# Optimization experiments

Measured on AMD Instinct MI355X. Metric: run time of the kernel, lower is better.

The kernel has to match this reference:

```python
import jax, jax.numpy as jnp
import numpy as np

B, L, N = 8, 5, 4096
RADIUS, K = 0.7, 32
SPATIAL_STRIDE = 16
TK, TSTRIDE = 3, 2  # temporal kernel / stride; temporal_padding=[1,1] replicate
DIM, DEPTH, HEADS, DIM_HEAD, MLP_DIM, OUT_DIM = 512, 5, 8, 64, 1024, 1088
INNER = HEADS * DIM_HEAD
N_ANCH = 64
NTOT = N + N_ANCH
M = NTOT // SPATIAL_STRIDE  # spatial anchors per output frame


def setup_inputs() -> dict:
    key = jax.random.key(0)
    ks = list(jax.random.split(key, 16))
    s = 0.02
    p = {}
    p["points"] = jax.random.uniform(ks[0], (B, L, N, 3), jnp.float32, -1.0, 1.0)
    p["conv_d_w"] = jax.random.normal(ks[1], (DIM, 4), jnp.float32) * s
    p["conv_f_w"] = jax.random.normal(ks[2], (DIM, 3), jnp.float32) * s
    p["pos_w"] = jax.random.normal(ks[3], (DIM, 4), jnp.float32) * s
    p["pos_b"] = jnp.zeros((DIM,), jnp.float32)
    p["ln1_g"] = jnp.ones((DEPTH, DIM)); p["ln1_b"] = jnp.zeros((DEPTH, DIM))
    p["qkv_w"] = jax.random.normal(ks[4], (DEPTH, DIM, 3 * INNER), jnp.float32) * s
    p["attn_out_w"] = jax.random.normal(ks[5], (DEPTH, INNER, DIM), jnp.float32) * s
    p["attn_out_b"] = jnp.zeros((DEPTH, DIM))
    p["ln2_g"] = jnp.ones((DEPTH, DIM)); p["ln2_b"] = jnp.zeros((DEPTH, DIM))
    p["ff1_w"] = jax.random.normal(ks[6], (DEPTH, DIM, MLP_DIM), jnp.float32) * s
    p["ff1_b"] = jnp.zeros((DEPTH, MLP_DIM))
    p["ff2_w"] = jax.random.normal(ks[7], (DEPTH, MLP_DIM, DIM), jnp.float32) * s
    p["ff2_b"] = jnp.zeros((DEPTH, DIM))
    p["head_ln_g"] = jnp.ones((DIM,)); p["head_ln_b"] = jnp.zeros((DIM,))
    p["head1_w"] = jax.random.normal(ks[8], (DIM, MLP_DIM), jnp.float32) * s
    p["head1_b"] = jnp.zeros((MLP_DIM,))
    p["head2_w"] = jax.random.normal(ks[9], (MLP_DIM, OUT_DIM), jnp.float32) * s
    p["head2_b"] = jnp.zeros((OUT_DIM,))
    return p


def _layer_norm(x, g, b, eps=1e-5):
    mu = jnp.mean(x, -1, keepdims=True)
    var = jnp.mean((x - mu) ** 2, -1, keepdims=True)
    return (x - mu) * jax.lax.rsqrt(var + eps) * g + b


def _anchor_grid():
    lin = jnp.linspace(-1.5, 1.5, 4)
    gx, gy, gz = jnp.meshgrid(lin, lin, lin, indexing="ij")
    return jnp.stack([gx.ravel(), gy.ravel(), gz.ravel()], -1)  # (64,3)


def _fps(pts, m):
    # furthest point sampling, pts (N,3) -> (m,) int32, first pick is index 0 (pointnet2 semantics)
    def step(carry, _):
        dist, last = carry
        d = jnp.sum((pts - pts[last]) ** 2, -1)
        dist = jnp.minimum(dist, d)
        return (dist, jnp.argmax(dist).astype(jnp.int32)), last
    init = (jnp.full((pts.shape[0],), 1e10, pts.dtype), jnp.int32(0))
    _, idx = jax.lax.scan(step, init, None, length=m)
    return idx


def _ball_query(anchors, pts, radius, k):
    # first k point indices within radius of each anchor; pad with first hit (0 if none)
    d2 = jnp.sum((anchors[:, None, :] - pts[None, :, :]) ** 2, -1)  # (M,N)
    n = pts.shape[0]
    cand = jnp.where(d2 < radius * radius, jnp.arange(n, dtype=jnp.int32), n)
    neg_topk, _ = jax.lax.top_k(-cand, k)  # k smallest indices, ascending
    idx = -neg_topk
    first = idx[:, :1]
    idx = jnp.where(idx == n, first, idx)
    return jnp.where(idx == n, 0, idx)


def _forward(points, conv_d_w, conv_f_w, pos_w, pos_b, ln1_g, ln1_b, qkv_w,
             attn_out_w, attn_out_b, ln2_g, ln2_b, ff1_w, ff1_b, ff2_w, ff2_b,
             head_ln_g, head_ln_b, head1_w, head1_b, head2_w, head2_b):
    anch = _anchor_grid()  # (64,3)
    pts = jnp.concatenate(
        [points[..., :3], jnp.broadcast_to(anch, (B, L, N_ANCH, 3))], axis=2)  # (B,L,NTOT,3)
    # replicate temporal padding [1,1]
    frames = jnp.concatenate([pts[:, :1], pts, pts[:, -1:]], axis=1)  # (B,L+2,NTOT,3)

    trad = (TK - 1) // 2
    nT = L + 2
    gather = jax.vmap(lambda p, i: p[i])
    out_xyz, out_feat = [], []
    for t in range(trad, nT - trad, TSTRIDE):
        f_t = frames[:, t]                                   # (B,NTOT,3)
        a_idx = jax.vmap(lambda p: _fps(p, M))(f_t)          # (B,M)
        a_xyz = gather(f_t, a_idx)                           # (B,M,3)
        feats_w = []
        for i in range(t - trad, t + trad + 1):
            nb = frames[:, i]                                # (B,NTOT,3)
            idx = jax.vmap(lambda a, p: _ball_query(a, p, RADIUS, K))(a_xyz, nb)  # (B,M,K)
            grouped = gather(nb, idx)                        # (B,M,K,3)
            disp = grouped - a_xyz[:, :, None, :]
            tdisp = jnp.full((B, M, K, 1), float(i - t), disp.dtype)
            disp4 = jnp.concatenate([disp, tdisp], -1)       # (B,M,K,4)
            # conv_f(features) + conv_d(displacement); features fed in are the xyz themselves
            feat = (jnp.einsum("bmkc,dc->bmkd", grouped, conv_f_w)
                    + jnp.einsum("bmkc,dc->bmkd", disp4, conv_d_w))
            feats_w.append(jnp.max(feat, axis=2))            # spatial max -> (B,M,DIM)
        out_feat.append(jnp.max(jnp.stack(feats_w, 0), axis=0))  # temporal max
        out_xyz.append(a_xyz)

    nF = len(out_xyz)
    xyzs = jnp.stack(out_xyz, 1)                             # (B,nF,M,3)
    feats = jnp.stack(out_feat, 1).reshape(B, nF * M, DIM)
    tcol = jnp.broadcast_to(
        jnp.arange(1, nF + 1, dtype=xyzs.dtype)[None, :, None, None], (B, nF, M, 1))
    xyzts = jnp.concatenate([xyzs, tcol], -1).reshape(B, nF * M, 4)
    x = jnp.einsum("bnc,dc->bnd", xyzts, pos_w) + pos_b + feats  # (B,T,DIM); emb_relu=False

    scale = DIM_HEAD ** -0.5
    for l in range(DEPTH):
        xn = _layer_norm(x, ln1_g[l], ln1_b[l])
        q, k, v = jnp.split(xn @ qkv_w[l], 3, axis=-1)
        rs = lambda a: a.reshape(B, -1, HEADS, DIM_HEAD)
        q, k, v = rs(q), rs(k), rs(v)
        att = jax.nn.softmax(jnp.einsum("bqhd,bkhd->bhqk", q, k) * scale, axis=-1)
        o = jnp.einsum("bhqk,bkhd->bqhd", att, v).reshape(B, -1, INNER)
        x = x + o @ attn_out_w[l] + attn_out_b[l]
        xn = _layer_norm(x, ln2_g[l], ln2_b[l])
        x = x + jax.nn.gelu(xn @ ff1_w[l] + ff1_b[l], approximate=False) @ ff2_w[l] + ff2_b[l]

    x = jnp.max(x, axis=1)                                   # (B,DIM)
    x = _layer_norm(x, head_ln_g, head_ln_b)
    x = jax.nn.gelu(x @ head1_w + head1_b, approximate=False) @ head2_w + head2_b
    x = x.reshape(B, 1, OUT_DIM // 64, 64)
    x = jax.nn.softmax(x, axis=-1)
    return x @ anch                                          # (B,1,J,3)


def reference(points, conv_d_w, conv_f_w, pos_w, pos_b, ln1_g, ln1_b, qkv_w,
              attn_out_w, attn_out_b, ln2_g, ln2_b, ff1_w, ff1_b, ff2_w, ff2_b,
              head_ln_g, head_ln_b, head1_w, head1_b, head2_w, head2_b):
    return _forward(points, conv_d_w, conv_f_w, pos_w, pos_b, ln1_g, ln1_b, qkv_w,
                    attn_out_w, attn_out_b, ln2_g, ln2_b, ff1_w, ff1_b, ff2_w, ff2_b,
                    head_ln_g, head_ln_b, head1_w, head1_b, head2_w, head2_b)
```

## Files before the change

### kernel.cpp

```cpp
#include <hip/hip_runtime.h>
#include <hip/hip_bf16.h>
#include <cstddef>

#define BB 8
#define LL 5
#define NN 4096
#define NANCH 64
#define NPTS 4160
#define MM 260
#define NFRAME 3
#define SSEQ 780
#define DIMC 512
#define NHEAD 8
#define DHEAD 64
#define MLPD 1024
#define OUTD 1088
#define NROWS 6240
#define VPITCH 784
#define WBUFSZ 2097152

typedef __attribute__((ext_vector_type(8))) short s16x8;
typedef __attribute__((ext_vector_type(4))) float fx4;
typedef unsigned short ushort_t;
typedef unsigned int uint_t;

__device__ __forceinline__ float sqdist_rn(float x1, float y1, float z1,
                                           float x2, float y2, float z2) {
    float dx = __fsub_rn(x1, x2);
    float dy = __fsub_rn(y1, y2);
    float dz = __fsub_rn(z1, z2);
    return __fadd_rn(__fadd_rn(__fmul_rn(dx, dx), __fmul_rn(dy, dy)), __fmul_rn(dz, dz));
}

__device__ __forceinline__ float gelu_exact(float v) {
    return 0.5f * v * (1.0f + erff(v * 0.70710678118654752440f));
}

__device__ __forceinline__ uint_t bf16rn(float f) {
    uint_t u = __float_as_uint(f);
    return (u + 0x7FFFu + ((u >> 16) & 1u)) >> 16;
}
__device__ __forceinline__ void split2(float f, ushort_t& h, ushort_t& l) {
    uint_t hb = bf16rn(f);
    h = (ushort_t)hb;
    float fh = __uint_as_float(hb << 16);
    l = (ushort_t)bf16rn(f - fh);
}

template <int CTRL>
__device__ __forceinline__ int dpp_mov(int v) {
    return __builtin_amdgcn_update_dpp(0, v, CTRL, 0xF, 0xF, true);
}
#define DPP_STEP_F(op, v, ctrl) v = op(v, __int_as_float(dpp_mov<ctrl>(__float_as_int(v))))
__device__ __forceinline__ float wave_max_bcast(float v) {
    DPP_STEP_F(fmaxf, v, 0x111); DPP_STEP_F(fmaxf, v, 0x112);
    DPP_STEP_F(fmaxf, v, 0x114); DPP_STEP_F(fmaxf, v, 0x118);
    DPP_STEP_F(fmaxf, v, 0x142); DPP_STEP_F(fmaxf, v, 0x143);
    return __int_as_float(__builtin_amdgcn_readlane(__float_as_int(v), 63));
}
__device__ __forceinline__ float faddf(float a, float b) { return a + b; }
__device__ __forceinline__ float wave_sum_bcast(float v) {
    DPP_STEP_F(faddf, v, 0x111); DPP_STEP_F(faddf, v, 0x112);
    DPP_STEP_F(faddf, v, 0x114); DPP_STEP_F(faddf, v, 0x118);
    DPP_STEP_F(faddf, v, 0x142); DPP_STEP_F(faddf, v, 0x143);
    return __int_as_float(__builtin_amdgcn_readlane(__float_as_int(v), 63));
}
#define DPP_STEP_I(v, ctrl) { int _x = dpp_mov<ctrl>(v); v = v > _x ? v : _x; }
__device__ __forceinline__ int wave_maxi_bcast(int v) {
    DPP_STEP_I(v, 0x111); DPP_STEP_I(v, 0x112);
    DPP_STEP_I(v, 0x114); DPP_STEP_I(v, 0x118);
    DPP_STEP_I(v, 0x142); DPP_STEP_I(v, 0x143);
    return __builtin_amdgcn_readlane(v, 63);
}
__device__ __forceinline__ float row16_maxf(float v) {
    DPP_STEP_F(fmaxf, v, 0x111); DPP_STEP_F(fmaxf, v, 0x112);
    DPP_STEP_F(fmaxf, v, 0x114); DPP_STEP_F(fmaxf, v, 0x118);
    return __int_as_float(__builtin_amdgcn_readlane(__float_as_int(v), 15));
}
__device__ __forceinline__ int row16_maxi(int v) {
    DPP_STEP_I(v, 0x111); DPP_STEP_I(v, 0x112);
    DPP_STEP_I(v, 0x114); DPP_STEP_I(v, 0x118);
    return __builtin_amdgcn_readlane(v, 15);
}

__device__ __forceinline__ void wsplit_tile(
    int bid, int tid, int nthr,
    const float* __restrict__ qkvw, const float* __restrict__ projw,
    const float* __restrict__ ff1w, const float* __restrict__ ff2w,
    ushort_t* __restrict__ th, ushort_t* __restrict__ tl,
    float (*T)[33]) {
    const float* src; int K, N; size_t dst;
    if (bid < 768)       { src = qkvw;  K = 512;  N = 1536; dst = 0;       }
    else if (bid < 1024) { src = projw; K = 512;  N = 512;  dst = 786432;  bid -= 768;  }
    else if (bid < 1536) { src = ff1w;  K = 512;  N = 1024; dst = 1048576; bid -= 1024; }
    else                 { src = ff2w;  K = 1024; N = 512;  dst = 1572864; bid -= 1536; }
    int ntn = N >> 5;
    int tn = bid % ntn, tk = bid / ntn;
    int n0 = tn * 32, k0 = tk * 32;
    for (int e = tid; e < 1024; e += nthr) {
        int r = e >> 5, c = e & 31;
        T[r][c] = src[(size_t)(k0 + r) * N + n0 + c];
    }
    __syncthreads();
    for (int e = tid; e < 1024; e += nthr) {
        int r = e >> 5, c = e & 31;
        ushort_t h, l;
        split2(T[c][r], h, l);
        th[dst + (size_t)(n0 + r) * K + k0 + c] = h;
        tl[dst + (size_t)(n0 + r) * K + k0 + c] = l;
    }
}

__global__ __launch_bounds__(256) void build_pts_kernel(const float* __restrict__ points,
                                                        float* __restrict__ pts) {
    int i = blockIdx.x * 256 + threadIdx.x;
    if (i >= BB * LL * NPTS) return;
    int n = i % NPTS;
    int bl = i / NPTS;
    if (n < NN) {
        const float* src = points + ((size_t)bl * NN + n) * 3;
        pts[(size_t)i * 3 + 0] = src[0];
        pts[(size_t)i * 3 + 1] = src[1];
        pts[(size_t)i * 3 + 2] = src[2];
    } else {
        int j = n - NN;
        int ix = j >> 4, iy = (j >> 2) & 3, iz = j & 3;
        pts[(size_t)i * 3 + 0] = -1.5f + (float)ix;
        pts[(size_t)i * 3 + 1] = -1.5f + (float)iy;
        pts[(size_t)i * 3 + 2] = -1.5f + (float)iz;
    }
}

__global__ __launch_bounds__(1024) void fps_ws_kernel(
    const float* __restrict__ pts, float* __restrict__ axyz,
    const float* __restrict__ qkvw, const float* __restrict__ projw,
    const float* __restrict__ ff1w, const float* __restrict__ ff2w,
    ushort_t* __restrict__ th, ushort_t* __restrict__ tl) {
    __shared__ __align__(16) char smem[50432];
    int bid = blockIdx.x;
    int tid = threadIdx.x;
    if (bid >= 24) {
        wsplit_tile(bid - 24, tid, 1024, qkvw, projw, ff1w, ff2w, th, tl,
                    (float(*)[33])smem);
        return;
    }
    float* sx = (float*)smem;
    float* sy = sx + NPTS;
    float* sz = sy + NPTS;
    float* redv = sz + NPTS;
    int* redi = (int*)(redv + 32);

    int b = bid / 3, f = bid % 3;
    const float* P = pts + (size_t)(b * LL + 2 * f) * NPTS * 3;
    int lane = tid & 63, wid = tid >> 6;
    const int PPT = 5;
    float px[PPT], py[PPT], pz[PPT], dist[PPT];
#pragma unroll
    for (int j = 0; j < PPT; j++) {
        int n = tid + 1024 * j;
        if (n < NPTS) {
            float gx = P[(size_t)n * 3 + 0];
            float gy = P[(size_t)n * 3 + 1];
            float gz = P[(size_t)n * 3 + 2];
            px[j] = gx; py[j] = gy; pz[j] = gz;
            sx[n] = gx; sy[n] = gy; sz[n] = gz;
            dist[j] = 1e10f;
        } else {
            px[j] = 0.f; py[j] = 0.f; pz[j] = 0.f;
            dist[j] = -1.0f;
        }
    }
    __syncthreads();
    float ax = sx[0], ay = sy[0], az = sz[0];
    float* out = axyz + (size_t)bid * MM * 3;
    for (int m = 0; m < MM; m++) {
        if (tid == 0) { out[m * 3 + 0] = ax; out[m * 3 + 1] = ay; out[m * 3 + 2] = az; }
        float bestv = -1.0f;
        int bestn = NPTS;
#pragma unroll
        for (int j = 0; j < PPT; j++) {
            int n = tid + 1024 * j;
            if (n < NPTS) {
                float d = sqdist_rn(px[j], py[j], pz[j], ax, ay, az);
                float dj = fminf(dist[j], d);
                dist[j] = dj;
                if (dj > bestv) { bestv = dj; bestn = n; }
            }
        }
        float wm = wave_max_bcast(bestv);
        int wn = 0x7FFFFFFF - wave_maxi_bcast(bestv == wm ? (0x7FFFFFFF - bestn) : 0);
        int par = (m & 1) * 16;
        if (lane == 0) { redv[par + wid] = wm; redi[par + wid] = wn; }
        __syncthreads();
        float cv = redv[par + (lane & 15)];
        int ci = redi[par + (lane & 15)];
        float bv = row16_maxf(cv);
        int bn = 0x7FFFFFFF - row16_maxi(cv == bv ? (0x7FFFFFFF - ci) : 0);
        ax = sx[bn]; ay = sy[bn]; az = sz[bn];
    }
}

__global__ __launch_bounds__(64) void group_conv_kernel(
    const float* __restrict__ pts, const float* __restrict__ axyz,
    const float* __restrict__ conv_d_w, const float* __restrict__ conv_f_w,
    const float* __restrict__ pos_w, const float* __restrict__ pos_b,
    float* __restrict__ x) {
    int gid = blockIdx.x;
    int b = gid / SSEQ;
    int rem = gid % SSEQ;
    int f = rem / MM;
    int lane = threadIdx.x;
    const float* A = axyz + (size_t)gid * 3;
    float ax = A[0], ay = A[1], az = A[2];

    float cf0[8], cf1[8], cf2[8], cd0[8], cd1[8], cd2[8], cd3[8], fmx[8];
#pragma unroll
    for (int c = 0; c < 8; c++) {
        int d = lane + 64 * c;
        cf0[c] = conv_f_w[d * 3 + 0];
        cf1[c] = conv_f_w[d * 3 + 1];
        cf2[c] = conv_f_w[d * 3 + 2];
        cd0[c] = conv_d_w[d * 4 + 0];
        cd1[c] = conv_d_w[d * 4 + 1];
        cd2[c] = conv_d_w[d * 4 + 2];
        cd3[c] = conv_d_w[d * 4 + 3];
        fmx[c] = -INFINITY;
    }
    __shared__ int nbr[32];
    __shared__ float gxs[32], gys[32], gzs[32];
    const float R2 = 0.49000000953674316f;

    for (int wi = 0; wi < 3; wi++) {
        int l = 2 * f + wi - 1;
        l = l < 0 ? 0 : (l > 4 ? 4 : l);
        const float* P = pts + (size_t)(b * LL + l) * NPTS * 3;
        int cnt = 0;
        for (int base = 0; base < NPTS && cnt < 32; base += 64) {
            int n = base + lane;
            float d2 = sqdist_rn(P[(size_t)n * 3], P[(size_t)n * 3 + 1], P[(size_t)n * 3 + 2],
                                 ax, ay, az);
            bool hit = d2 < R2;
            unsigned long long mk = __ballot(hit);
            int rank = (int)__popcll(mk & (((unsigned long long)1 << lane) - 1ull));
            if (hit && (cnt + rank) < 32) nbr[cnt + rank] = n;
            cnt += (int)__popcll(mk);
        }
        __syncthreads();
        int eff = cnt < 32 ? cnt : 32;
        if (lane < 32) {
            int idx = (eff == 0) ? 0 : (lane < eff ? nbr[lane] : nbr[0]);
            gxs[lane] = P[(size_t)idx * 3 + 0];
            gys[lane] = P[(size_t)idx * 3 + 1];
            gzs[lane] = P[(size_t)idx * 3 + 2];
        }
        __syncthreads();
        float tf = (float)(wi - 1);
        for (int k = 0; k < 32; k++) {
            float gx = gxs[k], gy = gys[k], gz = gzs[k];
            float dx = gx - ax, dy = gy - ay, dz = gz - az;
#pragma unroll
            for (int c = 0; c < 8; c++) {
                float v = gx * cf0[c] + gy * cf1[c] + gz * cf2[c] +
                          dx * cd0[c] + dy * cd1[c] + dz * cd2[c] + tf * cd3[c];
                fmx[c] = fmaxf(fmx[c], v);
            }
        }
        __syncthreads();
    }
    float tcol = (float)(f + 1);
#pragma unroll
    for (int c = 0; c < 8; c++) {
        int d = lane + 64 * c;
        float pos = ax * pos_w[d * 4 + 0] + ay * pos_w[d * 4 + 1] +
                    az * pos_w[d * 4 + 2] + tcol * pos_w[d * 4 + 3] + pos_b[d];
        x[(size_t)gid * DIMC + d] = fmx[c] + pos;
    }
}

__global__ __launch_bounds__(64) void ln_kernel(const float* __restrict__ x,
                                                const float* __restrict__ g,
                                                const float* __restrict__ b,
                                                ushort_t* __restrict__ yh,
                                                ushort_t* __restrict__ yl) {
    int r = blockIdx.x;
    int lane = threadIdx.x;
    const float* xr = x + (size_t)r * DIMC;
    float4 v0 = *(const float4*)(xr + lane * 8);
    float4 v1 = *(const float4*)(xr + lane * 8 + 4);
    float s = v0.x + v0.y + v0.z + v0.w + v1.x + v1.y + v1.z + v1.w;
    s = wave_sum_bcast(s);
    float mean = s * (1.0f / 512.0f);
    float dv[8];
    dv[0] = v0.x - mean; dv[1] = v0.y - mean; dv[2] = v0.z - mean; dv[3] = v0.w - mean;
    dv[4] = v1.x - mean; dv[5] = v1.y - mean; dv[6] = v1.z - mean; dv[7] = v1.w - mean;
    float sq = 0.f;
#pragma unroll
    for (int c = 0; c < 8; c++) sq += dv[c] * dv[c];
    sq = wave_sum_bcast(sq);
    float var = sq * (1.0f / 512.0f);
    float inv = 1.0f / sqrtf(var + 1e-5f);
    int d = lane * 8;
    ushort_t hs[8], ls[8];
#pragma unroll
    for (int c = 0; c < 8; c++) {
        float v = dv[c] * inv * g[d + c] + b[d + c];
        split2(v, hs[c], ls[c]);
    }
    uint4 hv, lv;
    hv.x = hs[0] | ((uint_t)hs[1] << 16); hv.y = hs[2] | ((uint_t)hs[3] << 16);
    hv.z = hs[4] | ((uint_t)hs[5] << 16); hv.w = hs[6] | ((uint_t)hs[7] << 16);
    lv.x = ls[0] | ((uint_t)ls[1] << 16); lv.y = ls[2] | ((uint_t)ls[3] << 16);
    lv.z = ls[4] | ((uint_t)ls[5] << 16); lv.w = ls[6] | ((uint_t)ls[7] << 16);
    *(uint4*)(yh + (size_t)r * DIMC + d) = hv;
    *(uint4*)(yl + (size_t)r * DIMC + d) = lv;
}

#define KP 40

template <int BN, int EPI>
__global__ __launch_bounds__(256, 2) void gemm_mfma(
    const ushort_t* __restrict__ Ahg, const ushort_t* __restrict__ Alg,
    const ushort_t* __restrict__ Bhg, const ushort_t* __restrict__ Blg,
    const float* __restrict__ bias, const float* __restrict__ R,
    float* __restrict__ C, ushort_t* __restrict__ Ch, ushort_t* __restrict__ Cl,
    ushort_t* __restrict__ Vh, ushort_t* __restrict__ Vl,
    int M, int N, int K) {
    const int WN = BN / 2, NT = WN / 16;
    __shared__ ushort_t Ah[128 * KP];
    __shared__ ushort_t Al[128 * KP];
    __shared__ ushort_t Bh[BN * KP];
    __shared__ ushort_t Bl[BN * KP];
    int tid = threadIdx.x;
    int lane = tid & 63, w = tid >> 6;
    int wm = w & 1, wn = w >> 1;
    int quad = lane >> 4, l15 = lane & 15;
    int m0 = blockIdx.y * 128, n0 = blockIdx.x * BN;

    int sa_row = tid >> 2;
    int sa_k = (tid & 3) * 8;

    int row_a0 = m0 + sa_row;       if (row_a0 >= M) row_a0 = M - 1;
    int row_a1 = m0 + sa_row + 64;  if (row_a1 >= M) row_a1 = M - 1;
    const ushort_t* pAh0 = Ahg + (size_t)row_a0 * K + sa_k;
    const ushort_t* pAl0 = Alg + (size_t)row_a0 * K + sa_k;
    const ushort_t* pAh1 = Ahg + (size_t)row_a1 * K + sa_k;
    const ushort_t* pAl1 = Alg + (size_t)row_a1 * K + sa_k;
    const ushort_t* pBh0 = Bhg + (size_t)(n0 + sa_row) * K + sa_k;
    const ushort_t* pBl0 = Blg + (size_t)(n0 + sa_row) * K + sa_k;
    const ushort_t* pBh1 = (BN == 128) ? Bhg + (size_t)(n0 + sa_row + 64) * K + sa_k : pBh0;
    const ushort_t* pBl1 = (BN == 128) ? Blg + (size_t)(n0 + sa_row + 64) * K + sa_k : pBl0;

    fx4 acc[4][NT];
#pragma unroll
    for (int mi = 0; mi < 4; mi++)
#pragma unroll
        for (int nj = 0; nj < NT; nj++) acc[mi][nj] = (fx4){0.f, 0.f, 0.f, 0.f};

    float4 ra0h = *(const float4*)pAh0, ra0l = *(const float4*)pAl0;
    float4 ra1h = *(const float4*)pAh1, ra1l = *(const float4*)pAl1;
    float4 rb0h = *(const float4*)pBh0, rb0l = *(const float4*)pBl0;
    float4 rb1h, rb1l;
    if (BN == 128) { rb1h = *(const float4*)pBh1; rb1l = *(const float4*)pBl1; }

    for (int k0 = 0; k0 < K; k0 += 32) {
        *(float4*)&Ah[sa_row * KP + sa_k] = ra0h;
        *(float4*)&Al[sa_row * KP + sa_k] = ra0l;
        *(float4*)&Ah[(sa_row + 64) * KP + sa_k] = ra1h;
        *(float4*)&Al[(sa_row + 64) * KP + sa_k] = ra1l;
        *(float4*)&Bh[sa_row * KP + sa_k] = rb0h;
        *(float4*)&Bl[sa_row * KP + sa_k] = rb0l;
        if (BN == 128) {
            *(float4*)&Bh[(sa_row + 64) * KP + sa_k] = rb1h;
            *(float4*)&Bl[(sa_row + 64) * KP + sa_k] = rb1l;
        }
        __syncthreads();
        int kn = k0 + 32;
        if (kn < K) {
            ra0h = *(const float4*)(pAh0 + kn); ra0l = *(const float4*)(pAl0 + kn);
            ra1h = *(const float4*)(pAh1 + kn); ra1l = *(const float4*)(pAl1 + kn);
            rb0h = *(const float4*)(pBh0 + kn); rb0l = *(const float4*)(pBl0 + kn);
            if (BN == 128) {
                rb1h = *(const float4*)(pBh1 + kn); rb1l = *(const float4*)(pBl1 + kn);
            }
        }
        s16x8 af[4][2], bf[NT][2];
#pragma unroll
        for (int mi = 0; mi < 4; mi++) {
            int off = (64 * wm + 16 * mi + l15) * KP + quad * 8;
            af[mi][0] = *(const s16x8*)&Ah[off];
            af[mi][1] = *(const s16x8*)&Al[off];
        }
#pragma unroll
        for (int nj = 0; nj < NT; nj++) {
            int off = (WN * wn + 16 * nj + l15) * KP + quad * 8;
            bf[nj][0] = *(const s16x8*)&Bh[off];
            bf[nj][1] = *(const s16x8*)&Bl[off];
        }
#pragma unroll
        for (int mi = 0; mi < 4; mi++)
#pragma unroll
            for (int nj = 0; nj < NT; nj++) {
                acc[mi][nj] = __builtin_amdgcn_mfma_f32_16x16x32_bf16(af[mi][0], bf[nj][0], acc[mi][nj], 0, 0, 0);
                acc[mi][nj] = __builtin_amdgcn_mfma_f32_16x16x32_bf16(af[mi][0], bf[nj][1], acc[mi][nj], 0, 0, 0);
                acc[mi][nj] = __builtin_amdgcn_mfma_f32_16x16x32_bf16(af[mi][1], bf[nj][0], acc[mi][nj], 0, 0, 0);
            }
        __syncthreads();
    }
#pragma unroll
    for (int mi = 0; mi < 4; mi++) {
#pragma unroll
        for (int r = 0; r < 4; r++) {
            int row = m0 + 64 * wm + 16 * mi + quad * 4 + r;
            if (row < M) {
#pragma unroll
                for (int nj = 0; nj < NT; nj++) {
                    int col = n0 + WN * wn + 16 * nj + l15;
                    float v = acc[mi][nj][r];
                    if (EPI == 0) {
                        C[(size_t)row * N + col] = v;
                    } else if (EPI == 3) {
                        C[(size_t)row * N + col] = v + bias[col] + R[(size_t)row * N + col];
                    } else if (EPI == 2) {
                        float gv = gelu_exact(v + bias[col]);
                        ushort_t h, l;
                        split2(gv, h, l);
                        Ch[(size_t)row * N + col] = h;
                        Cl[(size_t)row * N + col] = l;
                    } else if (EPI == 5) {
                        ushort_t h, l;
                        split2(v, h, l);
                        if (col < 1024) {
                            Ch[(size_t)row * 1024 + col] = h;
                            Cl[(size_t)row * 1024 + col] = l;
                        } else {
                            int bb = row / SSEQ, key = row % SSEQ;
                            int hh = (col - 1024) >> 6, dd = (col - 1024) & 63;
                            size_t vo = ((size_t)((bb * 8 + hh) * 64 + dd)) * VPITCH + key;
                            Vh[vo] = h;
                            Vl[vo] = l;
                        }
                    }
                }
            }
        }
    }
}

#define AP 72

__global__ __launch_bounds__(256, 2) void attn_mfma_kernel(
    const ushort_t* __restrict__ qkh, const ushort_t* __restrict__ qkl,
    const ushort_t* __restrict__ vth, const ushort_t* __restrict__ vtl,
    ushort_t* __restrict__ oh, ushort_t* __restrict__ ol,
    const float* __restrict__ nqkvw, const float* __restrict__ nprojw,
    const float* __restrict__ nff1w, const float* __restrict__ nff2w,
    ushort_t* __restrict__ nth, ushort_t* __restrict__ ntl) {
    __shared__ __align__(16) char smem[73728];
    if (blockIdx.x >= 13) {
        int widx = (blockIdx.x - 13) * 64 + blockIdx.y * 8 + blockIdx.z;
        wsplit_tile(widx, threadIdx.x, 256, nqkvw, nprojw, nff1w, nff2w,
                    nth, ntl, (float(*)[33])smem);
        return;
    }
    ushort_t* Qh  = (ushort_t*)smem;
    ushort_t* Ql  = Qh + 64 * AP;
    ushort_t* Kh  = Ql + 64 * AP;
    ushort_t* Kl  = Kh + 64 * AP;
    ushort_t* Vth = Kl + 64 * AP;
    ushort_t* Vtl = Vth + 64 * AP;
    ushort_t* Ph  = Vtl + 64 * AP;
    ushort_t* Pl  = Ph + 64 * AP;

    int qt = blockIdx.x, h = blockIdx.y, b = blockIdx.z;
    int tid = threadIdx.x;
    int lane = tid & 63, w = tid >> 6;
    int quad = lane >> 4, l15 = lane & 15;
    int bh = b * 8 + h;

    int q0 = qt * 64;
    int nq = SSEQ - q0; if (nq > 64) nq = 64;

#pragma unroll
    for (int i = 0; i < 2; i++) {
        int t = tid + 256 * i;
        int row = t >> 3, c = (t & 7) * 8;
        int gq = q0 + (row < nq ? row : nq - 1);
        size_t go = (size_t)(b * SSEQ + gq) * 1024 + h * 64 + c;
        *(uint4*)&Qh[row * AP + c] = *(const uint4*)(qkh + go);
        *(uint4*)&Ql[row * AP + c] = *(const uint4*)(qkl + go);
    }

    fx4 accO[4];
#pragma unroll
    for (int dj = 0; dj < 4; dj++) accO[dj] = (fx4){0.f, 0.f, 0.f, 0.f};
    fx4 accL = (fx4){0.f, 0.f, 0.f, 0.f};

    s16x8 ones;
#pragma unroll
    for (int j = 0; j < 8; j++) ones[j] = (short)16256;

    for (int kt = 0; kt < 13; kt++) {
        int k0 = kt * 64;
        int nk = SSEQ - k0; if (nk > 64) nk = 64;
        __syncthreads();
#pragma unroll
        for (int i = 0; i < 2; i++) {
            int t = tid + 256 * i;
            int row = t >> 3, c = (t & 7) * 8;
            int gk = k0 + (row < nk ? row : nk - 1);
            size_t go = (size_t)(b * SSEQ + gk) * 1024 + h * 64 + c;
            *(uint4*)&Kh[row * AP + c] = *(const uint4*)(qkh + go + 512);
            *(uint4*)&Kl[row * AP + c] = *(const uint4*)(qkl + go + 512);
            size_t vo = ((size_t)(bh * 64 + row)) * VPITCH + k0 + c;
            *(uint4*)&Vth[row * AP + c] = *(const uint4*)(vth + vo);
            *(uint4*)&Vtl[row * AP + c] = *(const uint4*)(vtl + vo);
        }
        __syncthreads();

        fx4 accS[4];
#pragma unroll
        for (int nj = 0; nj < 4; nj++) accS[nj] = (fx4){0.f, 0.f, 0.f, 0.f};
#pragma unroll
        for (int ks = 0; ks < 2; ks++) {
            s16x8 aH = *(const s16x8*)&Qh[(16 * w + l15) * AP + 32 * ks + quad * 8];
            s16x8 aL = *(const s16x8*)&Ql[(16 * w + l15) * AP + 32 * ks + quad * 8];
#pragma unroll
            for (int nj = 0; nj < 4; nj++) {
                s16x8 bH = *(const s16x8*)&Kh[(16 * nj + l15) * AP + 32 * ks + quad * 8];
                s16x8 bL = *(const s16x8*)&Kl[(16 * nj + l15) * AP + 32 * ks + quad * 8];
                accS[nj] = __builtin_amdgcn_mfma_f32_16x16x32_bf16(aH, bH, accS[nj], 0, 0, 0);
                accS[nj] = __builtin_amdgcn_mfma_f32_16x16x32_bf16(aH, bL, accS[nj], 0, 0, 0);
                accS[nj] = __builtin_amdgcn_mfma_f32_16x16x32_bf16(aL, bH, accS[nj], 0, 0, 0);
            }
        }
#pragma unroll
        for (int nj = 0; nj < 4; nj++) {
            int key = 16 * nj + l15;
            bool valid = key < nk;
#pragma unroll
            for (int r = 0; r < 4; r++) {
                float s = accS[nj][r] * 0.125f;
                float p = valid ? __expf(s) : 0.f;
                ushort_t hh, ll;
                split2(p, hh, ll);
                int qrow = 16 * w + quad * 4 + r;
                Ph[qrow * AP + key] = hh;
                Pl[qrow * AP + key] = ll;
            }
        }
#pragma unroll
        for (int ks = 0; ks < 2; ks++) {
            s16x8 aPh = *(const s16x8*)&Ph[(16 * w + l15) * AP + 32 * ks + quad * 8];
            s16x8 aPl = *(const s16x8*)&Pl[(16 * w + l15) * AP + 32 * ks + quad * 8];
            accL = __builtin_amdgcn_mfma_f32_16x16x32_bf16(aPh, ones, accL, 0, 0, 0);
            accL = __builtin_amdgcn_mfma_f32_16x16x32_bf16(aPl, ones, accL, 0, 0, 0);
#pragma unroll
            for (int dj = 0; dj < 4; dj++) {
                s16x8 bVh = *(const s16x8*)&Vth[(16 * dj + l15) * AP + 32 * ks + quad * 8];
                s16x8 bVl = *(const s16x8*)&Vtl[(16 * dj + l15) * AP + 32 * ks + quad * 8];
                accO[dj] = __builtin_amdgcn_mfma_f32_16x16x32_bf16(aPh, bVh, accO[dj], 0, 0, 0);
                accO[dj] = __builtin_amdgcn_mfma_f32_16x16x32_bf16(aPh, bVl, accO[dj], 0, 0, 0);
                accO[dj] = __builtin_amdgcn_mfma_f32_16x16x32_bf16(aPl, bVh, accO[dj], 0, 0, 0);
            }
        }
    }
#pragma unroll
    for (int r = 0; r < 4; r++) {
        int lq = 16 * w + quad * 4 + r;
        if (lq < nq) {
            float inv = 1.0f / accL[r];
            size_t base = (size_t)(b * SSEQ + q0 + lq) * DIMC + h * 64 + l15;
#pragma unroll
            for (int dj = 0; dj < 4; dj++) {
                ushort_t hh, ll;
                split2(accO[dj][r] * inv, hh, ll);
                oh[base + 16 * dj] = hh;
                ol[base + 16 * dj] = ll;
            }
        }
    }
}

__global__ __launch_bounds__(512) void pool_max_kernel(const float* __restrict__ x,
                                                       float* __restrict__ partial) {
    int c = blockIdx.x;
    int bb = blockIdx.y;
    int d = threadIdx.x;
    const float* xb = x + ((size_t)(bb * SSEQ + c * 60)) * DIMC + d;
    float m = -INFINITY;
#pragma unroll 4
    for (int s = 0; s < 60; s++) m = fmaxf(m, xb[(size_t)s * DIMC]);
    partial[((size_t)bb * 13 + c) * DIMC + d] = m;
}

__global__ __launch_bounds__(512) void pool_ln_kernel(const float* __restrict__ partial,
                                                      const float* __restrict__ g,
                                                      const float* __restrict__ b,
                                                      float* __restrict__ out) {
    int bb = blockIdx.x;
    int d = threadIdx.x;
    const float* pb = partial + (size_t)bb * 13 * DIMC + d;
    float m = -INFINITY;
#pragma unroll
    for (int c = 0; c < 13; c++) m = fmaxf(m, pb[(size_t)c * DIMC]);
    __shared__ float col[512];
    __shared__ float red[512];
    col[d] = m;
    red[d] = m;
    __syncthreads();
    for (int s = 256; s > 0; s >>= 1) {
        if (d < s) red[d] += red[d + s];
        __syncthreads();
    }
    float mean = red[0] * (1.0f / 512.0f);
    __syncthreads();
    float dv = col[d] - mean;
    red[d] = dv * dv;
    __syncthreads();
    for (int s = 256; s > 0; s >>= 1) {
        if (d < s) red[d] += red[d + s];
        __syncthreads();
    }
    float var = red[0] * (1.0f / 512.0f);
    float inv = 1.0f / sqrtf(var + 1e-5f);
    out[(size_t)bb * DIMC + d] = dv * inv * g[d] + b[d];
}

__global__ __launch_bounds__(256) void head1_kernel(const float* __restrict__ in,
                                                    const float* __restrict__ W,
                                                    const float* __restrict__ bias,
                                                    float* __restrict__ out) {
    int g = blockIdx.x, bb = blockIdx.y;
    int tid = threadIdx.x;
    int c = tid & 63, ks = tid >> 6;
    int col = g * 64 + c;
    __shared__ float xr[512];
    xr[tid] = in[(size_t)bb * 512 + tid];
    xr[tid + 256] = in[(size_t)bb * 512 + tid + 256];
    __syncthreads();
    float acc = 0.f;
    const float* Wc = W + col;
    for (int k = ks * 128; k < ks * 128 + 128; k++)
        acc += xr[k] * Wc[(size_t)k * MLPD];
    __shared__ float red[256];
    red[tid] = acc;
    __syncthreads();
    if (ks == 0) {
        float v = red[c] + red[c + 64] + red[c + 128] + red[c + 192] + bias[col];
        out[(size_t)bb * MLPD + col] = gelu_exact(v);
    }
}

__global__ __launch_bounds__(256) void head2_kernel(const float* __restrict__ in,
                                                    const float* __restrict__ W,
                                                    const float* __restrict__ bias,
                                                    float* __restrict__ out) {
    int g = blockIdx.x, bb = blockIdx.y;
    int tid = threadIdx.x;
    int c = tid & 63, ks = tid >> 6;
    int col = g * 64 + c;
    __shared__ float xr[1024];
    xr[tid] = in[(size_t)bb * 1024 + tid];
    xr[tid + 256] = in[(size_t)bb * 1024 + tid + 256];
    xr[tid + 512] = in[(size_t)bb * 1024 + tid + 512];
    xr[tid + 768] = in[(size_t)bb * 1024 + tid + 768];
    __syncthreads();
    float acc = 0.f;
    const float* Wc = W + col;
    for (int k = ks * 256; k < ks * 256 + 256; k++)
        acc += xr[k] * Wc[(size_t)k * OUTD];
    __shared__ float red[256];
    red[tid] = acc;
    __syncthreads();
    if (ks == 0) {
        out[(size_t)bb * OUTD + col] = red[c] + red[c + 64] + red[c + 128] + red[c + 192] + bias[col];
    }
}

__global__ __launch_bounds__(64) void smax_anchor_kernel(const float* __restrict__ h2,
                                                         float* __restrict__ out) {
    int bb = blockIdx.x / 17;
    int gcol = blockIdx.x % 17;
    int j = threadIdx.x;
    float v = h2[(size_t)bb * OUTD + gcol * 64 + j];
    float mx = wave_max_bcast(v);
    float p = expf(v - mx);
    float sum = wave_sum_bcast(p);
    int ix = j >> 4, iy = (j >> 2) & 3, iz = j & 3;
    float sx = wave_sum_bcast(p * (-1.5f + (float)ix));
    float sy = wave_sum_bcast(p * (-1.5f + (float)iy));
    float sz = wave_sum_bcast(p * (-1.5f + (float)iz));
    if (j == 0) {
        float* o = out + ((size_t)bb * 17 + gcol) * 3;
        o[0] = sx / sum;
        o[1] = sy / sum;
        o[2] = sz / sum;
    }
}

extern "C" void kernel_launch(void* const* d_in, const int* in_sizes, int n_in,
                              void* d_out, int out_size, void* d_ws, size_t ws_size,
                              hipStream_t stream) {
    const float* points     = (const float*)d_in[0];
    const float* conv_d_w   = (const float*)d_in[1];
    const float* conv_f_w   = (const float*)d_in[2];
    const float* pos_w      = (const float*)d_in[3];
    const float* pos_b      = (const float*)d_in[4];
    const float* ln1_g      = (const float*)d_in[5];
    const float* ln1_b      = (const float*)d_in[6];
    const float* qkv_w      = (const float*)d_in[7];
    const float* attn_out_w = (const float*)d_in[8];
    const float* attn_out_b = (const float*)d_in[9];
    const float* ln2_g      = (const float*)d_in[10];
    const float* ln2_b      = (const float*)d_in[11];
    const float* ff1_w      = (const float*)d_in[12];
    const float* ff1_b      = (const float*)d_in[13];
    const float* ff2_w      = (const float*)d_in[14];
    const float* ff2_b      = (const float*)d_in[15];
    const float* head_ln_g  = (const float*)d_in[16];
    const float* head_ln_b  = (const float*)d_in[17];
    const float* head1_w    = (const float*)d_in[18];
    const float* head1_b    = (const float*)d_in[19];
    const float* head2_w    = (const float*)d_in[20];
    const float* head2_b    = (const float*)d_in[21];

    float* ws = (float*)d_ws;
    float* pts    = ws;
    float* axyz   = pts + 499200;
    float* xbuf   = axyz + 18720;
    float* qkvreg = xbuf + 3194880;
    float* pooled = qkvreg + 9601024;
    float* h1     = pooled + 4096;
    float* h2     = h1 + 8192;
    float* fend   = h2 + 8704;
    ushort_t* qkh = (ushort_t*)qkvreg;
    ushort_t* qkl = qkh + 6389760;
    ushort_t* vth = qkl + 6389760;
    ushort_t* vtl = vth + 3211264;
    ushort_t* us   = (ushort_t*)fend;
    ushort_t* xnh  = us;
    ushort_t* xnl  = xnh + 3194880;
    ushort_t* atth = xnl + 3194880;
    ushort_t* attl = atth + 3194880;
    ushort_t* ffhh = attl + 3194880;
    ushort_t* ffhl = ffhh + 6389760;
    ushort_t* wbh  = ffhl + 6389760;
    ushort_t* wbl  = wbh + 2 * WBUFSZ;
    float* ppart = qkvreg;

    build_pts_kernel<<<650, 256, 0, stream>>>(points, pts);
    fps_ws_kernel<<<24 + 2048, 1024, 0, stream>>>(
        pts, axyz, qkv_w, attn_out_w, ff1_w, ff2_w, wbh, wbl);
    group_conv_kernel<<<NROWS, 64, 0, stream>>>(pts, axyz, conv_d_w, conv_f_w,
                                                pos_w, pos_b, xbuf);
    const int MB = (NROWS + 127) / 128;
    for (int l = 0; l < 5; l++) {
        ushort_t* wth = wbh + (size_t)(l & 1) * WBUFSZ;
        ushort_t* wtl = wbl + (size_t)(l & 1) * WBUFSZ;
        ushort_t* nth = wbh + (size_t)((l + 1) & 1) * WBUFSZ;
        ushort_t* ntl = wbl + (size_t)((l + 1) & 1) * WBUFSZ;
        int ln2off = l * 512;
        ln_kernel<<<NROWS, 64, 0, stream>>>(xbuf, ln1_g + ln2off, ln1_b + ln2off, xnh, xnl);
        gemm_mfma<128, 5><<<dim3(1536 / 128, MB), 256, 0, stream>>>(
            xnh, xnl, wth, wtl, nullptr, nullptr, nullptr, qkh, qkl, vth, vtl,
            NROWS, 1536, 512);
        int lnx = l + 1;
        attn_mfma_kernel<<<dim3(l < 4 ? 45 : 13, NHEAD, BB), 256, 0, stream>>>(
            qkh, qkl, vth, vtl, atth, attl,
            l < 4 ? qkv_w + (size_t)lnx * 512 * 1536 : nullptr,
            l < 4 ? attn_out_w + (size_t)lnx * 512 * 512 : nullptr,
            l < 4 ? ff1_w + (size_t)lnx * 512 * 1024 : nullptr,
            l < 4 ? ff2_w + (size_t)lnx * 1024 * 512 : nullptr,
            nth, ntl);
        gemm_mfma<64, 3><<<dim3(512 / 64, MB), 256, 0, stream>>>(
            atth, attl, wth + 786432, wtl + 786432, attn_out_b + ln2off, xbuf,
            xbuf, nullptr, nullptr, nullptr, nullptr, NROWS, 512, 512);
        ln_kernel<<<NROWS, 64, 0, stream>>>(xbuf, ln2_g + ln2off, ln2_b + ln2off, xnh, xnl);
        gemm_mfma<128, 2><<<dim3(1024 / 128, MB), 256, 0, stream>>>(
            xnh, xnl, wth + 1048576, wtl + 1048576, ff1_b + l * 1024, nullptr,
            nullptr, ffhh, ffhl, nullptr, nullptr, NROWS, 1024, 512);
        gemm_mfma<64, 3><<<dim3(512 / 64, MB), 256, 0, stream>>>(
            ffhh, ffhl, wth + 1572864, wtl + 1572864, ff2_b + ln2off, xbuf,
            xbuf, nullptr, nullptr, nullptr, nullptr, NROWS, 512, 1024);
    }
    pool_max_kernel<<<dim3(13, BB), 512, 0, stream>>>(xbuf, ppart);
    pool_ln_kernel<<<BB, 512, 0, stream>>>(ppart, head_ln_g, head_ln_b, pooled);
    head1_kernel<<<dim3(16, BB), 256, 0, stream>>>(pooled, head1_w, head1_b, h1);
    head2_kernel<<<dim3(17, BB), 256, 0, stream>>>(h1, head2_w, head2_b, h2);
    smax_anchor_kernel<<<BB * 17, 64, 0, stream>>>(h2, (float*)d_out);
}
```

Baseline: 2.010 ms.

## Load GEMM tiles directly into LDS with swizzle and simplify FPS argmax

The GEMM mainloop now uses global_load_lds to copy A/B tiles straight into shared memory with an XOR swizzle. This replaces the register-staged prefetch and the padded KP layout, but it drops the software prefetch overlap because the loads are now synchronous with the barrier. The FPS kernel switches to contiguous per-thread point ranges and finds the argmax with ballot/ffs/readlane instead of a second integer DPP reduction. That shortens the serial 260-step loop, though tie-breaking now depends on the contiguous index ordering.

```diff
diff --git a/kernel.cpp b/kernel.cpp
--- a/kernel.cpp
+++ b/kernel.cpp
@@ -47,6 +47,12 @@
     l = (ushort_t)bf16rn(f - fh);
 }
 
+typedef __attribute__((address_space(3))) unsigned int as3u;
+typedef const __attribute__((address_space(1))) unsigned int as1u;
+__device__ __forceinline__ void gload16(const ushort_t* g, ushort_t* l) {
+    __builtin_amdgcn_global_load_lds((as1u*)g, (as3u*)l, 16, 0, 0);
+}
+
 template <int CTRL>
 __device__ __forceinline__ int dpp_mov(int v) {
     return __builtin_amdgcn_update_dpp(0, v, CTRL, 0xF, 0xF, true);
@@ -65,22 +71,10 @@
     DPP_STEP_F(faddf, v, 0x142); DPP_STEP_F(faddf, v, 0x143);
     return __int_as_float(__builtin_amdgcn_readlane(__float_as_int(v), 63));
 }
-#define DPP_STEP_I(v, ctrl) { int _x = dpp_mov<ctrl>(v); v = v > _x ? v : _x; }
-__device__ __forceinline__ int wave_maxi_bcast(int v) {
-    DPP_STEP_I(v, 0x111); DPP_STEP_I(v, 0x112);
-    DPP_STEP_I(v, 0x114); DPP_STEP_I(v, 0x118);
-    DPP_STEP_I(v, 0x142); DPP_STEP_I(v, 0x143);
-    return __builtin_amdgcn_readlane(v, 63);
-}
 __device__ __forceinline__ float row16_maxf(float v) {
     DPP_STEP_F(fmaxf, v, 0x111); DPP_STEP_F(fmaxf, v, 0x112);
     DPP_STEP_F(fmaxf, v, 0x114); DPP_STEP_F(fmaxf, v, 0x118);
     return __int_as_float(__builtin_amdgcn_readlane(__float_as_int(v), 15));
-}
-__device__ __forceinline__ int row16_maxi(int v) {
-    DPP_STEP_I(v, 0x111); DPP_STEP_I(v, 0x112);
-    DPP_STEP_I(v, 0x114); DPP_STEP_I(v, 0x118);
-    return __builtin_amdgcn_readlane(v, 15);
 }
 
 __device__ __forceinline__ void wsplit_tile(
@@ -153,12 +147,13 @@
     int b = bid / 3, f = bid % 3;
     const float* P = pts + (size_t)(b * LL + 2 * f) * NPTS * 3;
     int lane = tid & 63, wid = tid >> 6;
-    const int PPT = 5;
-    float px[PPT], py[PPT], pz[PPT], dist[PPT];
-#pragma unroll
-    for (int j = 0; j < PPT; j++) {
-        int n = tid + 1024 * j;
-        if (n < NPTS) {
+    int start = tid < 64 ? 5 * tid : 320 + 4 * (tid - 64);
+    int cnt = tid < 64 ? 5 : 4;
+    float px[5], py[5], pz[5], dist[5];
+#pragma unroll
+    for (int j = 0; j < 5; j++) {
+        if (j < cnt) {
+            int n = start + j;
             float gx = P[(size_t)n * 3 + 0];
             float gy = P[(size_t)n * 3 + 1];
             float gz = P[(size_t)n * 3 + 2];
@@ -175,27 +170,37 @@
     float* out = axyz + (size_t)bid * MM * 3;
     for (int m = 0; m < MM; m++) {
         if (tid == 0) { out[m * 3 + 0] = ax; out[m * 3 + 1] = ay; out[m * 3 + 2] = az; }
-        float bestv = -1.0f;
-        int bestn = NPTS;
-#pragma unroll
-        for (int j = 0; j < PPT; j++) {
-            int n = tid + 1024 * j;
-            if (n < NPTS) {
-                float d = sqdist_rn(px[j], py[j], pz[j], ax, ay, az);
-                float dj = fminf(dist[j], d);
-                dist[j] = dj;
-                if (dj > bestv) { bestv = dj; bestn = n; }
-            }
-        }
-        float wm = wave_max_bcast(bestv);
-        int wn = 0x7FFFFFFF - wave_maxi_bcast(bestv == wm ? (0x7FFFFFFF - bestn) : 0);
+        float bv = -1.0f;
+#pragma unroll
+        for (int j = 0; j < 4; j++) {
+            float d = sqdist_rn(px[j], py[j], pz[j], ax, ay, az);
+            float dj = fminf(dist[j], d);
+            dist[j] = dj;
+            bv = fmaxf(bv, dj);
+        }
+        if (cnt == 5) {
+            float d = sqdist_rn(px[4], py[4], pz[4], ax, ay, az);
+            float dj = fminf(dist[4], d);
+            dist[4] = dj;
+            bv = fmaxf(bv, dj);
+        }
+        float wmv = wave_max_bcast(bv);
+        unsigned long long mk = __ballot(bv == wmv);
+        int srcl = __ffsll(mk) - 1;
+        int fn = start;
+#pragma unroll
+        for (int j = 4; j >= 0; j--)
+            if (dist[j] == wmv) fn = start + j;
+        int wn = __builtin_amdgcn_readlane(fn, srcl);
         int par = (m & 1) * 16;
-        if (lane == 0) { redv[par + wid] = wm; redi[par + wid] = wn; }
+        if (lane == 0) { redv[par + wid] = wmv; redi[par + wid] = wn; }
         __syncthreads();
         float cv = redv[par + (lane & 15)];
         int ci = redi[par + (lane & 15)];
-        float bv = row16_maxf(cv);
-        int bn = 0x7FFFFFFF - row16_maxi(cv == bv ? (0x7FFFFFFF - ci) : 0);
+        float bw = row16_maxf(cv);
+        unsigned long long mk2 = __ballot(cv == bw);
+        int w16 = __ffsll(mk2) - 1;
+        int bn = __builtin_amdgcn_readlane(ci, w16);
         ax = sx[bn]; ay = sy[bn]; az = sz[bn];
     }
 }
@@ -315,10 +320,10 @@
     *(uint4*)(yl + (size_t)r * DIMC + d) = lv;
 }
 
-#define KP 40
+#define BK 32
 
 template <int BN, int EPI>
-__global__ __launch_bounds__(256, 2) void gemm_mfma(
+__global__ __launch_bounds__(256) void gemm_mfma(
     const ushort_t* __restrict__ Ahg, const ushort_t* __restrict__ Alg,
     const ushort_t* __restrict__ Bhg, const ushort_t* __restrict__ Blg,
     const float* __restrict__ bias, const float* __restrict__ R,
@@ -326,29 +331,37 @@
     ushort_t* __restrict__ Vh, ushort_t* __restrict__ Vl,
     int M, int N, int K) {
     const int WN = BN / 2, NT = WN / 16;
-    __shared__ ushort_t Ah[128 * KP];
-    __shared__ ushort_t Al[128 * KP];
-    __shared__ ushort_t Bh[BN * KP];
-    __shared__ ushort_t Bl[BN * KP];
+    __shared__ __align__(16) ushort_t Ah[128 * BK];
+    __shared__ __align__(16) ushort_t Al[128 * BK];
+    __shared__ __align__(16) ushort_t Bh[BN * BK];
+    __shared__ __align__(16) ushort_t Bl[BN * BK];
     int tid = threadIdx.x;
     int lane = tid & 63, w = tid >> 6;
     int wm = w & 1, wn = w >> 1;
     int quad = lane >> 4, l15 = lane & 15;
     int m0 = blockIdx.y * 128, n0 = blockIdx.x * BN;
 
-    int sa_row = tid >> 2;
-    int sa_k = (tid & 3) * 8;
-
-    int row_a0 = m0 + sa_row;       if (row_a0 >= M) row_a0 = M - 1;
-    int row_a1 = m0 + sa_row + 64;  if (row_a1 >= M) row_a1 = M - 1;
-    const ushort_t* pAh0 = Ahg + (size_t)row_a0 * K + sa_k;
-    const ushort_t* pAl0 = Alg + (size_t)row_a0 * K + sa_k;
-    const ushort_t* pAh1 = Ahg + (size_t)row_a1 * K + sa_k;
-    const ushort_t* pAl1 = Alg + (size_t)row_a1 * K + sa_k;
-    const ushort_t* pBh0 = Bhg + (size_t)(n0 + sa_row) * K + sa_k;
-    const ushort_t* pBl0 = Blg + (size_t)(n0 + sa_row) * K + sa_k;
-    const ushort_t* pBh1 = (BN == 128) ? Bhg + (size_t)(n0 + sa_row + 64) * K + sa_k : pBh0;
-    const ushort_t* pBl1 = (BN == 128) ? Blg + (size_t)(n0 + sa_row + 64) * K + sa_k : pBl0;
+    int sr = lane >> 2;
+    int sc = lane & 3;
+    int kq = ((sc ^ ((sr >> 1) & 3)) << 3);
+
+    int aoff[2];
+#pragma unroll
+    for (int i = 0; i < 2; i++) {
+        int g = w + 4 * i;
+        int row = m0 + g * 16 + sr; if (row >= M) row = M - 1;
+        aoff[i] = row * K + kq;
+    }
+    int boff[BN == 128 ? 2 : 1];
+    if (BN == 128) {
+#pragma unroll
+        for (int i = 0; i < 2; i++) {
+            int g = w + 4 * i;
+            boff[i] = (n0 + g * 16 + sr) * K + kq;
+        }
+    } else {
+        boff[0] = (n0 + w * 16 + sr) * K + kq;
+    }
 
     fx4 acc[4][NT];
 #pragma unroll
@@ -356,54 +369,47 @@
 #pragma unroll
         for (int nj = 0; nj < NT; nj++) acc[mi][nj] = (fx4){0.f, 0.f, 0.f, 0.f};
 
-    float4 ra0h = *(const float4*)pAh0, ra0l = *(const float4*)pAl0;
-    float4 ra1h = *(const float4*)pAh1, ra1l = *(const float4*)pAl1;
-    float4 rb0h = *(const float4*)pBh0, rb0l = *(const float4*)pBl0;
-    float4 rb1h, rb1l;
-    if (BN == 128) { rb1h = *(const float4*)pBh1; rb1l = *(const float4*)pBl1; }
-
-    for (int k0 = 0; k0 < K; k0 += 32) {
-        *(float4*)&Ah[sa_row * KP + sa_k] = ra0h;
-        *(float4*)&Al[sa_row * KP + sa_k] = ra0l;
-        *(float4*)&Ah[(sa_row + 64) * KP + sa_k] = ra1h;
-        *(float4*)&Al[(sa_row + 64) * KP + sa_k] = ra1l;
-        *(float4*)&Bh[sa_row * KP + sa_k] = rb0h;
-        *(float4*)&Bl[sa_row * KP + sa_k] = rb0l;
+    int rsw = (l15 >> 1) & 3;
+    int aro = (64 * wm + l15) * BK + ((quad ^ rsw) << 3);
+    int bro = (WN * wn + l15) * BK + ((quad ^ rsw) << 3);
+
+    for (int k0 = 0; k0 < K; k0 += BK) {
+#pragma unroll
+        for (int i = 0; i < 2; i++) {
+            int g = w + 4 * i;
+            gload16(Ahg + aoff[i] + k0, &Ah[g * 16 * BK]);
+            gload16(Alg + aoff[i] + k0, &Al[g * 16 * BK]);
+        }
         if (BN == 128) {
-            *(float4*)&Bh[(sa_row + 64) * KP + sa_k] = rb1h;
-            *(float4*)&Bl[(sa_row + 64) * KP + sa_k] = rb1l;
-        }
-        __syncthreads();
-        int kn = k0 + 32;
-        if (kn < K) {
-            ra0h = *(const float4*)(pAh0 + kn); ra0l = *(const float4*)(pAl0 + kn);
-            ra1h = *(const float4*)(pAh1 + kn); ra1l = *(const float4*)(pAl1 + kn);
-            rb0h = *(const float4*)(pBh0 + kn); rb0l = *(const float4*)(pBl0 + kn);
-            if (BN == 128) {
-                rb1h = *(const float4*)(pBh1 + kn); rb1l = *(const float4*)(pBl1 + kn);
+#pragma unroll
+            for (int i = 0; i < 2; i++) {
+                int g = w + 4 * i;
+                gload16(Bhg + boff[i] + k0, &Bh[g * 16 * BK]);
+                gload16(Blg + boff[i] + k0, &Bl[g * 16 * BK]);
             }
-        }
-        s16x8 af[4][2], bf[NT][2];
+        } else {
+            gload16(Bhg + boff[0] + k0, &Bh[w * 16 * BK]);
+            gload16(Blg + boff[0] + k0, &Bl[w * 16 * BK]);
+        }
+        __syncthreads();
+
+        s16x8 bf[NT][2];
+#pragma unroll
+        for (int nj = 0; nj < NT; nj++) {
+            bf[nj][0] = *(const s16x8*)&Bh[bro + 16 * nj * BK];
+            bf[nj][1] = *(const s16x8*)&Bl[bro + 16 * nj * BK];
+        }
 #pragma unroll
         for (int mi = 0; mi < 4; mi++) {
-            int off = (64 * wm + 16 * mi + l15) * KP + quad * 8;
-            af[mi][0] = *(const s16x8*)&Ah[off];
-            af[mi][1] = *(const s16x8*)&Al[off];
-        }
-#pragma unroll
-        for (int nj = 0; nj < NT; nj++) {
-            int off = (WN * wn + 16 * nj + l15) * KP + quad * 8;
-            bf[nj][0] = *(const s16x8*)&Bh[off];
-            bf[nj][1] = *(const s16x8*)&Bl[off];
-        }
-#pragma unroll
-        for (int mi = 0; mi < 4; mi++)
+            s16x8 aH = *(const s16x8*)&Ah[aro + 16 * mi * BK];
+            s16x8 aL = *(const s16x8*)&Al[aro + 16 * mi * BK];
 #pragma unroll
             for (int nj = 0; nj < NT; nj++) {
-                acc[mi][nj] = __builtin_amdgcn_mfma_f32_16x16x32_bf16(af[mi][0], bf[nj][0], acc[mi][nj], 0, 0, 0);
-                acc[mi][nj] = __builtin_amdgcn_mfma_f32_16x16x32_bf16(af[mi][0], bf[nj][1], acc[mi][nj], 0, 0, 0);
-                acc[mi][nj] = __builtin_amdgcn_mfma_f32_16x16x32_bf16(af[mi][1], bf[nj][0], acc[mi][nj], 0, 0, 0);
+                acc[mi][nj] = __builtin_amdgcn_mfma_f32_16x16x32_bf16(aH, bf[nj][0], acc[mi][nj], 0, 0, 0);
+                acc[mi][nj] = __builtin_amdgcn_mfma_f32_16x16x32_bf16(aH, bf[nj][1], acc[mi][nj], 0, 0, 0);
+                acc[mi][nj] = __builtin_amdgcn_mfma_f32_16x16x32_bf16(aL, bf[nj][0], acc[mi][nj], 0, 0, 0);
             }
+        }
         __syncthreads();
     }
 #pragma unroll
```

New measurement: 1.987 ms. Within noise of the previous version (-1.1%).
